# Kernel tuning notes

Hardware: AMD Instinct MI355X
Metric: run time of the kernel (lower is better)

Reference implementation:

```python
import jax, jax.numpy as jnp
import numpy as np

N = 4096
STD = 0.01


def setup_inputs() -> dict:
    key = jax.random.key(0)
    ks = jax.random.split(key, 16)
    p = lambda k, shape: STD * jax.random.normal(k, shape, dtype=jnp.float32)
    return {
        "t": 0,
        "x": jax.random.normal(ks[0], (N, 1), dtype=jnp.float32),
        "A": jax.random.normal(ks[1], (N, N), dtype=jnp.float32),
        # MLP_A: 2 -> 16 -> 16 -> 1 (ReLU between hidden layers), torch (out,in) layout
        "WA0": p(ks[2], (16, 2)), "bA0": p(ks[3], (16,)),
        "WA1": p(ks[4], (16, 16)), "bA1": p(ks[5], (16,)),
        "WA2": p(ks[6], (1, 16)), "bA2": p(ks[7], (1,)),
        # MLP: 1 -> 16 -> 1 (ReLU after first layer)
        "Wm0": p(ks[8], (16, 1)), "bm0": p(ks[9], (16,)),
        "Wm1": p(ks[10], (1, 16)), "bm1": p(ks[11], (1,)),
        # linear_A: 2 -> 1, no bias; linear_f: 1 -> 1, no bias
        "wA": p(ks[12], (1, 2)),
        "wf": p(ks[13], (1, 1)),
    }


def reference(t, x, A, WA0, bA0, WA1, bA1, WA2, bA2, Wm0, bm0, Wm1, bm1, wA, wf):
    n = x.shape[0]
    # node MLP branch: hidden_list[0] == 1 != 0
    x_N = jax.nn.relu(x @ Wm0.T + bm0) @ Wm1.T + bm1 + x @ wf.T  # (n, 1)
    # all-pairs features: x_a[i, j] = (x_i, x_j)
    x1 = jnp.broadcast_to(x, (n, n))       # row i = x_i repeated
    x2 = jnp.broadcast_to(x.T, (n, n))     # row i = full x vector
    x_a = jnp.stack((x1, x2), axis=-1)     # (n, n, 2)
    # edge MLP (2 -> 16 -> 16 -> 1) + skip linear_A (2 -> 1)
    h = jax.nn.relu(x_a @ WA0.T + bA0)     # (n, n, 16)
    h = jax.nn.relu(h @ WA1.T + bA1)       # (n, n, 16)
    x_e = (h @ WA2.T + bA2)[..., 0]        # (n, n)
    x_12 = (x_a @ wA.T)[..., 0]            # (n, n)
    # adjacency-weighted reduction over neighbors (dim=1)
    x_A = jnp.sum(A * (x_e + x_12), axis=1, keepdims=True)  # (n, 1)
    return x_N + x_A
```

## Files before the change

### kernel.cpp

```cpp
#include <hip/hip_runtime.h>
#include <hip/hip_bf16.h>


#define NN 4096

typedef __fp16 half8  __attribute__((ext_vector_type(8)));
typedef __fp16 half2v __attribute__((ext_vector_type(2)));
typedef __attribute__((ext_vector_type(4)))  float f32x4;
typedef __attribute__((ext_vector_type(16))) float f32x16;

__device__ __forceinline__ half2v cvt2(float lo, float hi) {
    return __builtin_amdgcn_cvt_pkrtz(lo, hi);
}

__global__ __launch_bounds__(256, 4) void odef_kernel(
    const float* __restrict__ x,  const float* __restrict__ A,
    const float* __restrict__ WA0, const float* __restrict__ bA0,
    const float* __restrict__ WA1, const float* __restrict__ bA1,
    const float* __restrict__ WA2, const float* __restrict__ bA2,
    const float* __restrict__ Wm0, const float* __restrict__ bm0,
    const float* __restrict__ Wm1, const float* __restrict__ bm1,
    const float* __restrict__ wA,  const float* __restrict__ wf,
    float* __restrict__ out)
{
    __shared__ float xs[NN];
    __shared__ float ring[4][4][256];

    const int tid  = threadIdx.x;
    const int wave = tid >> 6;
    const int lane = tid & 63;
    const int n    = lane & 31;
    const int half = lane >> 5;
    const int row  = blockIdx.x * 4 + wave;

    {
        const f32x4* xsrc = (const f32x4*)x;
        f32x4* xdst = (f32x4*)xs;
        #pragma unroll
        for (int i = 0; i < 4; ++i)
            xdst[tid + 256 * i] = xsrc[tid + 256 * i];
    }

    const float xi = x[row];
    const float* arow = A + (size_t)row * NN;

    auto issue = [&](int pair) {
        const float* src = arow + pair * 256 + lane * 4;
        __builtin_amdgcn_global_load_lds(
            (const __attribute__((address_space(1))) void*)src,
            (__attribute__((address_space(3))) void*)&ring[wave][pair & 3][0],
            16, 0, 0);
    };

    issue(0); issue(1); issue(2);

    union { half2v h2[4]; half8 h8; } au;
    #pragma unroll
    for (int p = 0; p < 4; ++p) {
        float lo = 0.f, hi = 0.f;
        if (n < 16) {
            int k = half * 8 + p * 2;
            lo = WA1[n * 16 + k];
            hi = WA1[n * 16 + k + 1];
        }
        au.h2[p] = cvt2(lo, hi);
    }

    half2v u2h[4], w2h[4];
    #pragma unroll
    for (int p = 0; p < 4; ++p) {
        int k0 = half * 8 + p * 2;
        u2h[p] = cvt2(fmaf(WA0[2 * k0],     xi, bA0[k0]),
                      fmaf(WA0[2 * k0 + 2], xi, bA0[k0 + 1]));
        w2h[p] = cvt2(WA0[2 * k0 + 1], WA0[2 * k0 + 3]);
    }

    half2v wa2h[4], bb[4];
    #pragma unroll
    for (int p = 0; p < 4; ++p) {
        int r  = 2 * p;
        int m0 = (r & 3) + 8 * (r >> 2) + 4 * half;
        wa2h[p] = cvt2(WA2[m0], WA2[m0 + 1]);
        bb[p]   = cvt2(bA1[m0], bA1[m0 + 1]);
    }

    const float wA1h = half ? 0.f : wA[1];
    const float c0h  = half ? 0.f : (bA2[0] + wA[0] * xi);
    const half2v z2 = { (__fp16)0.f, (__fp16)0.f };
    const f32x16 zc = {};

    float acc0 = 0.f, acc1 = 0.f;

    auto body = [&](const f32x4 xv, const f32x4 av) {
        #pragma unroll
        for (int q = 0; q < 4; q += 2) {
            half2v xg0 = cvt2(xv[q], xv[q]);
            union { half2v h2[4]; half8 h8; } b0;
            #pragma unroll
            for (int p = 0; p < 4; ++p)
                b0.h2[p] = __builtin_elementwise_max(w2h[p] * xg0 + u2h[p], z2);
            f32x16 d0 = __builtin_amdgcn_mfma_f32_32x32x16_f16(au.h8, b0.h8, zc, 0, 0, 0);

            half2v xg1 = cvt2(xv[q + 1], xv[q + 1]);
            union { half2v h2[4]; half8 h8; } b1;
            #pragma unroll
            for (int p = 0; p < 4; ++p)
                b1.h2[p] = __builtin_elementwise_max(w2h[p] * xg1 + u2h[p], z2);
            f32x16 d1 = __builtin_amdgcn_mfma_f32_32x32x16_f16(au.h8, b1.h8, zc, 0, 0, 0);

            {
                float pp = fmaf(wA1h, xv[q], c0h);
                #pragma unroll
                for (int p = 0; p < 4; ++p) {
                    half2v t = __builtin_elementwise_max(
                        cvt2(d0[2 * p], d0[2 * p + 1]) + bb[p], z2);
                    pp = __builtin_amdgcn_fdot2(t, wa2h[p], pp, false);
                }
                acc0 = fmaf(av[q], pp, acc0);
            }
            {
                float pp = fmaf(wA1h, xv[q + 1], c0h);
                #pragma unroll
                for (int p = 0; p < 4; ++p) {
                    half2v t = __builtin_elementwise_max(
                        cvt2(d1[2 * p], d1[2 * p + 1]) + bb[p], z2);
                    pp = __builtin_amdgcn_fdot2(t, wa2h[p], pp, false);
                }
                acc1 = fmaf(av[q + 1], pp, acc1);
            }
        }
    };

    __syncthreads();

    const f32x4* xls = (const f32x4*)xs;
    f32x4 xv = xls[n];

#define STEP(P, WN, DO_ISSUE)                                                \
    {                                                                        \
        if (DO_ISSUE) issue((P) + 3);                                        \
        asm volatile("s_waitcnt vmcnt(" #WN ")" ::: "memory");               \
        __builtin_amdgcn_sched_barrier(0);                                   \
        const f32x4* sp = (const f32x4*)&ring[wave][(P) & 3][0];             \
        f32x4 av0 = sp[n];                                                   \
        f32x4 av1 = sp[32 + n];                                              \
        f32x4 xn0 = xls[(2 * (P) + 1) * 32 + n];                             \
        f32x4 xn1 = ((P) < 15) ? xls[(2 * (P) + 2) * 32 + n] : xn0;          \
        body(xv, av0);                                                       \
        body(xn0, av1);                                                      \
        xv = xn1;                                                            \
    }

    for (int P = 0; P < 13; ++P)
        STEP(P, 3, true);
    STEP(13, 2, false);
    STEP(14, 1, false);
    STEP(15, 0, false);
#undef STEP

    float acc = acc0 + acc1;
    #pragma unroll
    for (int off = 32; off > 0; off >>= 1)
        acc += __shfl_xor(acc, off);

    if (lane == 0) {
        float xn = fmaf(wf[0], xi, bm1[0]);
        #pragma unroll
        for (int h = 0; h < 16; ++h)
            xn = fmaf(Wm1[h], fmaxf(fmaf(Wm0[h], xi, bm0[h]), 0.f), xn);
        out[row] = xn + acc;
    }
}

extern "C" void kernel_launch(void* const* d_in, const int* in_sizes, int n_in,
                              void* d_out, int out_size, void* d_ws, size_t ws_size,
                              hipStream_t stream) {
    const float* x   = (const float*)d_in[1];
    const float* A   = (const float*)d_in[2];
    const float* WA0 = (const float*)d_in[3];
    const float* bA0 = (const float*)d_in[4];
    const float* WA1 = (const float*)d_in[5];
    const float* bA1 = (const float*)d_in[6];
    const float* WA2 = (const float*)d_in[7];
    const float* bA2 = (const float*)d_in[8];
    const float* Wm0 = (const float*)d_in[9];
    const float* bm0 = (const float*)d_in[10];
    const float* Wm1 = (const float*)d_in[11];
    const float* bm1 = (const float*)d_in[12];
    const float* wA  = (const float*)d_in[13];
    const float* wf  = (const float*)d_in[14];
    float* out = (float*)d_out;

    odef_kernel<<<NN / 4, 256, 0, stream>>>(x, A, WA0, bA0, WA1, bA1, WA2, bA2,
                                            Wm0, bm0, Wm1, bm1, wA, wf, out);
}
```

Measured before the change: 142.7 us.

## Stream A rows directly into registers with an 8-deep load pipeline

```diff
diff --git a/kernel.cpp b/kernel.cpp
--- a/kernel.cpp
+++ b/kernel.cpp
@@ -24,7 +24,6 @@
     float* __restrict__ out)
 {
     __shared__ float xs[NN];
-    __shared__ float ring[4][4][256];
 
     const int tid  = threadIdx.x;
     const int wave = tid >> 6;
@@ -40,19 +39,7 @@
         for (int i = 0; i < 4; ++i)
             xdst[tid + 256 * i] = xsrc[tid + 256 * i];
     }
-
     const float xi = x[row];
-    const float* arow = A + (size_t)row * NN;
-
-    auto issue = [&](int pair) {
-        const float* src = arow + pair * 256 + lane * 4;
-        __builtin_amdgcn_global_load_lds(
-            (const __attribute__((address_space(1))) void*)src,
-            (__attribute__((address_space(3))) void*)&ring[wave][pair & 3][0],
-            16, 0, 0);
-    };
-
-    issue(0); issue(1); issue(2);
 
     union { half2v h2[4]; half8 h8; } au;
     #pragma unroll
@@ -133,30 +120,56 @@
 
     __syncthreads();
 
+    const float* ap = A + (size_t)row * NN + 4 * n;
     const f32x4* xls = (const f32x4*)xs;
-    f32x4 xv = xls[n];
-
-#define STEP(P, WN, DO_ISSUE)                                                \
-    {                                                                        \
-        if (DO_ISSUE) issue((P) + 3);                                        \
-        asm volatile("s_waitcnt vmcnt(" #WN ")" ::: "memory");               \
-        __builtin_amdgcn_sched_barrier(0);                                   \
-        const f32x4* sp = (const f32x4*)&ring[wave][(P) & 3][0];             \
-        f32x4 av0 = sp[n];                                                   \
-        f32x4 av1 = sp[32 + n];                                              \
-        f32x4 xn0 = xls[(2 * (P) + 1) * 32 + n];                             \
-        f32x4 xn1 = ((P) < 15) ? xls[(2 * (P) + 2) * 32 + n] : xn0;          \
-        body(xv, av0);                                                       \
-        body(xn0, av1);                                                      \
-        xv = xn1;                                                            \
-    }
-
-    for (int P = 0; P < 13; ++P)
-        STEP(P, 3, true);
-    STEP(13, 2, false);
-    STEP(14, 1, false);
-    STEP(15, 0, false);
-#undef STEP
+
+#define LOADA(dst, p) \
+    asm volatile("global_load_dwordx4 %0, %1, off" : "=v"(dst) : "v"(p))
+#define WAITV(N) do {                                              \
+    asm volatile("s_waitcnt vmcnt(" #N ")" ::: "memory");          \
+    __builtin_amdgcn_sched_barrier(0); } while (0)
+
+    __builtin_amdgcn_sched_barrier(0);
+    asm volatile("s_waitcnt vmcnt(0)" ::: "memory");
+    __builtin_amdgcn_sched_barrier(0);
+
+    f32x4 L0,  L1,  L2,  L3,  L4,  L5,  L6,  L7,
+          L8,  L9,  L10, L11, L12, L13, L14, L15,
+          L16, L17, L18, L19, L20, L21, L22, L23,
+          L24, L25, L26, L27, L28, L29, L30, L31;
+
+    LOADA(L0, ap + 128 * 0);  LOADA(L1, ap + 128 * 1);
+    LOADA(L2, ap + 128 * 2);  LOADA(L3, ap + 128 * 3);
+    LOADA(L4, ap + 128 * 4);  LOADA(L5, ap + 128 * 5);
+    LOADA(L6, ap + 128 * 6);  LOADA(L7, ap + 128 * 7);
+
+#define STEPM(T, CUR, NXT) {                                       \
+        f32x4 xv = xls[n + 32 * (T)];                              \
+        WAITV(7);                                                  \
+        body(xv, CUR);                                             \
+        LOADA(NXT, ap + 128 * ((T) + 8)); }
+
+    STEPM(0,  L0,  L8)   STEPM(1,  L1,  L9)   STEPM(2,  L2,  L10)
+    STEPM(3,  L3,  L11)  STEPM(4,  L4,  L12)  STEPM(5,  L5,  L13)
+    STEPM(6,  L6,  L14)  STEPM(7,  L7,  L15)  STEPM(8,  L8,  L16)
+    STEPM(9,  L9,  L17)  STEPM(10, L10, L18)  STEPM(11, L11, L19)
+    STEPM(12, L12, L20)  STEPM(13, L13, L21)  STEPM(14, L14, L22)
+    STEPM(15, L15, L23)  STEPM(16, L16, L24)  STEPM(17, L17, L25)
+    STEPM(18, L18, L26)  STEPM(19, L19, L27)  STEPM(20, L20, L28)
+    STEPM(21, L21, L29)  STEPM(22, L22, L30)  STEPM(23, L23, L31)
+
+#define STEPT(T, WN, CUR) {                                        \
+        f32x4 xv = xls[n + 32 * (T)];                              \
+        WAITV(WN);                                                 \
+        body(xv, CUR); }
+
+    STEPT(24, 7, L24) STEPT(25, 6, L25) STEPT(26, 5, L26) STEPT(27, 4, L27)
+    STEPT(28, 3, L28) STEPT(29, 2, L29) STEPT(30, 1, L30) STEPT(31, 0, L31)
+
+#undef STEPM
+#undef STEPT
+#undef LOADA
+#undef WAITV
 
     float acc = acc0 + acc1;
     #pragma unroll
```

Result: no change. 145.3 us (+1.8%).
